# Performance work log

Hardware: AMD Instinct MI355X
Metric: run time of the kernel (lower is better)

The kernel has to match this reference:

```python
import jax, jax.numpy as jnp
import numpy as np

B, H, W, C = 16, 256, 256, 16
HO, WO = 256, 256


def setup_inputs() -> dict:
    key = jax.random.key(0)
    k1, k2 = jax.random.split(key)
    x = jax.random.normal(k1, (B, H, W, C), dtype=jnp.float32)
    # loc network: global avg pool -> dense(C, 6); small weights, identity bias
    W_loc = jax.random.normal(k2, (C, 6), dtype=jnp.float32) * 0.01
    b_loc = jnp.asarray([1.0, 0.0, 0.0, 1.0, 0.0, 0.0], dtype=jnp.float32)
    # coords_grid = np.indices(output_grid_shape): (2, HO, WO), [0]=row idx, [1]=col idx
    coords_grid = jnp.asarray(np.indices((HO, WO), dtype=np.float32))
    return {"x": x, "W_loc": W_loc, "b_loc": b_loc, "coords_grid": coords_grid}


def _forward(x, W_loc, b_loc, coords_grid):
    # loc network: predict 6 affine params per batch element
    pooled = jnp.mean(x, axis=(1, 2))              # [B, C]
    params = pooled @ W_loc + b_loc                # [B, 6]
    A = params[:, :4].reshape(-1, 2, 2)            # [B, 2, 2]
    t = params[:, 4:]                              # [B, 2]
    # grid_transform_fn: affine map of pixel coordinates
    tc = jnp.einsum('bij,jhw->bihw', A, coords_grid) + t[:, :, None, None]  # [B,2,HO,WO]
    yc, xc = tc[:, 0], tc[:, 1]                    # [B, HO, WO] each
    # interpolation_fn: bilinear sampling with clipping (wrap=False)
    y0 = jnp.floor(yc)
    x0 = jnp.floor(xc)
    wy = yc - y0                                   # fractional weights
    wx = xc - x0
    y0i = jnp.clip(y0.astype(jnp.int32), 0, H - 1)
    y1i = jnp.clip(y0.astype(jnp.int32) + 1, 0, H - 1)
    x0i = jnp.clip(x0.astype(jnp.int32), 0, W - 1)
    x1i = jnp.clip(x0.astype(jnp.int32) + 1, 0, W - 1)
    bidx = jnp.arange(x.shape[0])[:, None, None]   # [B,1,1] batch gather index
    Ia = x[bidx, y0i, x0i]                         # [B,HO,WO,C]
    Ib = x[bidx, y0i, x1i]
    Ic = x[bidx, y1i, x0i]
    Id = x[bidx, y1i, x1i]
    wa = ((1.0 - wy) * (1.0 - wx))[..., None]
    wb = ((1.0 - wy) * wx)[..., None]
    wc = (wy * (1.0 - wx))[..., None]
    wd = (wy * wx)[..., None]
    return wa * Ia + wb * Ib + wc * Ic + wd * Id   # [B,HO,WO,C]


def reference(x, W_loc, b_loc, coords_grid):
    return _forward(x, W_loc, b_loc, coords_grid)
```

## Files before the change

kernel.cpp:

```cpp
#include <hip/hip_runtime.h>

#define BB 16
#define HH 256
#define WW 256
#define CC 16
#define NPIX (HH * WW)
#define SLICES 128
#define POOL_BLOCKS (BB * SLICES)
#define SAMPLE_BPB 128
#define SAMPLE_BLOCKS (BB * SAMPLE_BPB)

__global__ __launch_bounds__(256) void pool_partial(const float4* __restrict__ x4,
                                                    float4* __restrict__ part) {
    const int blk = blockIdx.x;
    const int tid = threadIdx.x;
    const float4* p = x4 + (size_t)blk * 2048 + tid;
    float4 acc = {0.f, 0.f, 0.f, 0.f};
#pragma unroll
    for (int k = 0; k < 8; ++k) {
        float4 v = p[k * 256];
        acc.x += v.x; acc.y += v.y; acc.z += v.z; acc.w += v.w;
    }
    for (int off = 4; off < 64; off <<= 1) {
        acc.x += __shfl_down(acc.x, off);
        acc.y += __shfl_down(acc.y, off);
        acc.z += __shfl_down(acc.z, off);
        acc.w += __shfl_down(acc.w, off);
    }
    __shared__ float4 wsum[4][4];
    const int wave = tid >> 6, lane = tid & 63;
    if (lane < 4) wsum[wave][lane] = acc;
    __syncthreads();
    if (tid < 4) {
        float4 t0 = wsum[0][tid], t1 = wsum[1][tid];
        float4 t2 = wsum[2][tid], t3 = wsum[3][tid];
        float4 t;
        t.x = t0.x + t1.x + t2.x + t3.x;
        t.y = t0.y + t1.y + t2.y + t3.y;
        t.z = t0.z + t1.z + t2.z + t3.z;
        t.w = t0.w + t1.w + t2.w + t3.w;
        part[blk * 4 + tid] = t;
    }
}

__global__ __launch_bounds__(256) void sample_fused(
    const float4* __restrict__ x4,
    const float* __restrict__ W_loc,
    const float* __restrict__ b_loc,
    const float4* __restrict__ part,
    float4* __restrict__ out)
{
    const int tid  = threadIdx.x;
    const int blk  = blockIdx.x;
    const int b    = blk >> 7;
    const int wave = tid >> 6, lane = tid & 63;

    __shared__ float4 wsum[4][4];
    __shared__ float  pooled[CC];
    __shared__ float  pr[6];

    {
        const float4* q = part + (size_t)b * 512;
        float4 a0 = q[tid], a1 = q[tid + 256];
        float4 acc;
        acc.x = a0.x + a1.x; acc.y = a0.y + a1.y;
        acc.z = a0.z + a1.z; acc.w = a0.w + a1.w;
        for (int off = 4; off < 64; off <<= 1) {
            acc.x += __shfl_down(acc.x, off);
            acc.y += __shfl_down(acc.y, off);
            acc.z += __shfl_down(acc.z, off);
            acc.w += __shfl_down(acc.w, off);
        }
        if (lane < 4) wsum[wave][lane] = acc;
        __syncthreads();
        if (tid < 4) {
            float4 t0 = wsum[0][tid], t1 = wsum[1][tid];
            float4 t2 = wsum[2][tid], t3 = wsum[3][tid];
            pooled[tid * 4 + 0] = (t0.x + t1.x + t2.x + t3.x) * (1.0f / 65536.0f);
            pooled[tid * 4 + 1] = (t0.y + t1.y + t2.y + t3.y) * (1.0f / 65536.0f);
            pooled[tid * 4 + 2] = (t0.z + t1.z + t2.z + t3.z) * (1.0f / 65536.0f);
            pooled[tid * 4 + 3] = (t0.w + t1.w + t2.w + t3.w) * (1.0f / 65536.0f);
        }
        __syncthreads();
        if (tid < 6) {
            float a = b_loc[tid];
#pragma unroll
            for (int c = 0; c < CC; ++c)
                a += pooled[c] * W_loc[c * 6 + tid];
            pr[tid] = a;
        }
        __syncthreads();
    }

    const float p0 = pr[0], p1 = pr[1], p2 = pr[2];
    const float p3 = pr[3], p4 = pr[4], p5 = pr[5];
    const size_t base    = (size_t)b * NPIX;
    const int    pixBase = (blk & 127) * 512 + (tid >> 2);
    const int    cq      = tid & 3;

#pragma unroll 4
    for (int k = 0; k < 8; ++k) {
        const int pix = pixBase + k * 64;
        const int h = pix >> 8;
        const int w = pix & 255;

        const float fh = (float)h, fw = (float)w;
        const float yc = p0 * fh + p1 * fw + p4;
        const float xc = p2 * fh + p3 * fw + p5;

        const float y0f = floorf(yc), x0f = floorf(xc);
        const float wy = yc - y0f, wx = xc - x0f;
        const int y0 = (int)y0f, x0 = (int)x0f;
        const int y0i = min(max(y0, 0), HH - 1);
        const int y1i = min(max(y0 + 1, 0), HH - 1);
        const int x0i = min(max(x0, 0), WW - 1);
        const int x1i = min(max(x0 + 1, 0), WW - 1);

        const float4* r0 = x4 + (base + (size_t)y0i * WW) * 4 + cq;
        const float4* r1 = x4 + (base + (size_t)y1i * WW) * 4 + cq;
        const float4 Ia = r0[(size_t)x0i * 4];
        const float4 Ib = r0[(size_t)x1i * 4];
        const float4 Ic = r1[(size_t)x0i * 4];
        const float4 Id = r1[(size_t)x1i * 4];

        const float wa = (1.f - wy) * (1.f - wx);
        const float wb = (1.f - wy) * wx;
        const float wc = wy * (1.f - wx);
        const float wd = wy * wx;

        float4 o;
        o.x = wa * Ia.x + wb * Ib.x + wc * Ic.x + wd * Id.x;
        o.y = wa * Ia.y + wb * Ib.y + wc * Ic.y + wd * Id.y;
        o.z = wa * Ia.z + wb * Ib.z + wc * Ic.z + wd * Id.z;
        o.w = wa * Ia.w + wb * Ib.w + wc * Ic.w + wd * Id.w;

        out[(base + pix) * 4 + cq] = o;
    }
}

extern "C" void kernel_launch(void* const* d_in, const int* in_sizes, int n_in,
                              void* d_out, int out_size, void* d_ws, size_t ws_size,
                              hipStream_t stream) {
    const float* x     = (const float*)d_in[0];
    const float* W_loc = (const float*)d_in[1];
    const float* b_loc = (const float*)d_in[2];

    float4* part = (float4*)d_ws;

    pool_partial<<<POOL_BLOCKS, 256, 0, stream>>>((const float4*)x, part);
    sample_fused<<<SAMPLE_BLOCKS, 256, 0, stream>>>((const float4*)x, W_loc, b_loc,
                                                    part, (float4*)d_out);
}
```

Baseline: 129.9 us.

## Stage source rows in LDS for bilinear sampling when row span is small

Each sampling block covers two output rows. It now computes the range of input rows those rows map to, and when the range is at most four rows it copies them into 64KB of dynamic LDS with coalesced loads, then gathers the four taps from LDS instead of global memory. Blocks with a wider range keep the old global-gather path. This adds an extra sync and a large LDS allocation that limits occupancy, and the launch bounds now ask for two blocks per CU. With near-identity transforms the staged rows closely match rows the gathers would hit anyway, so the saving over L2-cached gathers may be small.

```diff
diff --git a/kernel.cpp b/kernel.cpp
--- a/kernel.cpp
+++ b/kernel.cpp
@@ -9,6 +9,7 @@
 #define POOL_BLOCKS (BB * SLICES)
 #define SAMPLE_BPB 128
 #define SAMPLE_BLOCKS (BB * SAMPLE_BPB)
+#define MAXR 4
 
 __global__ __launch_bounds__(256) void pool_partial(const float4* __restrict__ x4,
                                                     float4* __restrict__ part) {
@@ -43,21 +44,23 @@
     }
 }
 
-__global__ __launch_bounds__(256) void sample_fused(
+__global__ __launch_bounds__(256, 2) void sample_fused(
     const float4* __restrict__ x4,
     const float* __restrict__ W_loc,
     const float* __restrict__ b_loc,
     const float4* __restrict__ part,
     float4* __restrict__ out)
 {
+    extern __shared__ float lds_f[];
+    float4* ldsRows = (float4*)lds_f;
+    float4* wsum    = (float4*)lds_f;
+    float*  pooled  = lds_f + 64;
+    float*  prs     = lds_f + 80;
+
     const int tid  = threadIdx.x;
     const int blk  = blockIdx.x;
     const int b    = blk >> 7;
     const int wave = tid >> 6, lane = tid & 63;
-
-    __shared__ float4 wsum[4][4];
-    __shared__ float  pooled[CC];
-    __shared__ float  pr[6];
 
     {
         const float4* q = part + (size_t)b * 512;
@@ -71,11 +74,11 @@
             acc.z += __shfl_down(acc.z, off);
             acc.w += __shfl_down(acc.w, off);
         }
-        if (lane < 4) wsum[wave][lane] = acc;
+        if (lane < 4) wsum[wave * 4 + lane] = acc;
         __syncthreads();
         if (tid < 4) {
-            float4 t0 = wsum[0][tid], t1 = wsum[1][tid];
-            float4 t2 = wsum[2][tid], t3 = wsum[3][tid];
+            float4 t0 = wsum[0 * 4 + tid], t1 = wsum[1 * 4 + tid];
+            float4 t2 = wsum[2 * 4 + tid], t3 = wsum[3 * 4 + tid];
             pooled[tid * 4 + 0] = (t0.x + t1.x + t2.x + t3.x) * (1.0f / 65536.0f);
             pooled[tid * 4 + 1] = (t0.y + t1.y + t2.y + t3.y) * (1.0f / 65536.0f);
             pooled[tid * 4 + 2] = (t0.z + t1.z + t2.z + t3.z) * (1.0f / 65536.0f);
@@ -87,54 +90,113 @@
 #pragma unroll
             for (int c = 0; c < CC; ++c)
                 a += pooled[c] * W_loc[c * 6 + tid];
-            pr[tid] = a;
-        }
-        __syncthreads();
-    }
-
-    const float p0 = pr[0], p1 = pr[1], p2 = pr[2];
-    const float p3 = pr[3], p4 = pr[4], p5 = pr[5];
+            prs[tid] = a;
+        }
+        __syncthreads();
+    }
+
+    const float p0 = prs[0], p1 = prs[1], p2 = prs[2];
+    const float p3 = prs[3], p4 = prs[4], p5 = prs[5];
+    __syncthreads();
+
     const size_t base    = (size_t)b * NPIX;
-    const int    pixBase = (blk & 127) * 512 + (tid >> 2);
+    const int    local   = blk & 127;
+    const int    h0      = local * 2;
+    const int    pixBase = local * 512 + (tid >> 2);
     const int    cq      = tid & 3;
 
+    const float yc00 = p0 * (float)h0       + p4;
+    const float yc01 = p0 * (float)h0       + p1 * 255.f + p4;
+    const float yc10 = p0 * (float)(h0 + 1) + p4;
+    const float yc11 = p0 * (float)(h0 + 1) + p1 * 255.f + p4;
+    const float ymn = fminf(fminf(yc00, yc01), fminf(yc10, yc11));
+    const float ymx = fmaxf(fmaxf(yc00, yc01), fmaxf(yc10, yc11));
+    const int y_lo = min(max((int)floorf(ymn), 0), HH - 1);
+    const int y_hi = min(max((int)floorf(ymx) + 1, 0), HH - 1);
+    const int NR   = y_hi - y_lo + 1;
+
+    if (NR <= MAXR) {
+        const float4* src = x4 + (base + (size_t)y_lo * WW) * 4;
+        const int nf4 = NR * 1024;
+        for (int i = tid; i < nf4; i += 256)
+            ldsRows[i] = src[i];
+        __syncthreads();
+
 #pragma unroll 4
-    for (int k = 0; k < 8; ++k) {
-        const int pix = pixBase + k * 64;
-        const int h = pix >> 8;
-        const int w = pix & 255;
-
-        const float fh = (float)h, fw = (float)w;
-        const float yc = p0 * fh + p1 * fw + p4;
-        const float xc = p2 * fh + p3 * fw + p5;
-
-        const float y0f = floorf(yc), x0f = floorf(xc);
-        const float wy = yc - y0f, wx = xc - x0f;
-        const int y0 = (int)y0f, x0 = (int)x0f;
-        const int y0i = min(max(y0, 0), HH - 1);
-        const int y1i = min(max(y0 + 1, 0), HH - 1);
-        const int x0i = min(max(x0, 0), WW - 1);
-        const int x1i = min(max(x0 + 1, 0), WW - 1);
-
-        const float4* r0 = x4 + (base + (size_t)y0i * WW) * 4 + cq;
-        const float4* r1 = x4 + (base + (size_t)y1i * WW) * 4 + cq;
-        const float4 Ia = r0[(size_t)x0i * 4];
-        const float4 Ib = r0[(size_t)x1i * 4];
-        const float4 Ic = r1[(size_t)x0i * 4];
-        const float4 Id = r1[(size_t)x1i * 4];
-
-        const float wa = (1.f - wy) * (1.f - wx);
-        const float wb = (1.f - wy) * wx;
-        const float wc = wy * (1.f - wx);
-        const float wd = wy * wx;
-
-        float4 o;
-        o.x = wa * Ia.x + wb * Ib.x + wc * Ic.x + wd * Id.x;
-        o.y = wa * Ia.y + wb * Ib.y + wc * Ic.y + wd * Id.y;
-        o.z = wa * Ia.z + wb * Ib.z + wc * Ic.z + wd * Id.z;
-        o.w = wa * Ia.w + wb * Ib.w + wc * Ic.w + wd * Id.w;
-
-        out[(base + pix) * 4 + cq] = o;
+        for (int k = 0; k < 8; ++k) {
+            const int pix = pixBase + k * 64;
+            const int h = pix >> 8;
+            const int w = pix & 255;
+
+            const float fh = (float)h, fw = (float)w;
+            const float yc = p0 * fh + p1 * fw + p4;
+            const float xc = p2 * fh + p3 * fw + p5;
+
+            const float y0f = floorf(yc), x0f = floorf(xc);
+            const float wy = yc - y0f, wx = xc - x0f;
+            const int y0 = (int)y0f, x0 = (int)x0f;
+            const int s0  = min(max(y0, 0), HH - 1) - y_lo;
+            const int s1  = min(max(y0 + 1, 0), HH - 1) - y_lo;
+            const int x0i = min(max(x0, 0), WW - 1);
+            const int x1i = min(max(x0 + 1, 0), WW - 1);
+
+            const float4 Ia = ldsRows[s0 * 1024 + x0i * 4 + cq];
+            const float4 Ib = ldsRows[s0 * 1024 + x1i * 4 + cq];
+            const float4 Ic = ldsRows[s1 * 1024 + x0i * 4 + cq];
+            const float4 Id = ldsRows[s1 * 1024 + x1i * 4 + cq];
+
+            const float wa = (1.f - wy) * (1.f - wx);
+            const float wb = (1.f - wy) * wx;
+            const float wc = wy * (1.f - wx);
+            const float wd = wy * wx;
+
+            float4 o;
+            o.x = wa * Ia.x + wb * Ib.x + wc * Ic.x + wd * Id.x;
+            o.y = wa * Ia.y + wb * Ib.y + wc * Ic.y + wd * Id.y;
+            o.z = wa * Ia.z + wb * Ib.z + wc * Ic.z + wd * Id.z;
+            o.w = wa * Ia.w + wb * Ib.w + wc * Ic.w + wd * Id.w;
+
+            out[(base + pix) * 4 + cq] = o;
+        }
+    } else {
+#pragma unroll 4
+        for (int k = 0; k < 8; ++k) {
+            const int pix = pixBase + k * 64;
+            const int h = pix >> 8;
+            const int w = pix & 255;
+
+            const float fh = (float)h, fw = (float)w;
+            const float yc = p0 * fh + p1 * fw + p4;
+            const float xc = p2 * fh + p3 * fw + p5;
+
+            const float y0f = floorf(yc), x0f = floorf(xc);
+            const float wy = yc - y0f, wx = xc - x0f;
+            const int y0 = (int)y0f, x0 = (int)x0f;
+            const int y0i = min(max(y0, 0), HH - 1);
+            const int y1i = min(max(y0 + 1, 0), HH - 1);
+            const int x0i = min(max(x0, 0), WW - 1);
+            const int x1i = min(max(x0 + 1, 0), WW - 1);
+
+            const float4* r0 = x4 + (base + (size_t)y0i * WW) * 4 + cq;
+            const float4* r1 = x4 + (base + (size_t)y1i * WW) * 4 + cq;
+            const float4 Ia = r0[(size_t)x0i * 4];
+            const float4 Ib = r0[(size_t)x1i * 4];
+            const float4 Ic = r1[(size_t)x0i * 4];
+            const float4 Id = r1[(size_t)x1i * 4];
+
+            const float wa = (1.f - wy) * (1.f - wx);
+            const float wb = (1.f - wy) * wx;
+            const float wc = wy * (1.f - wx);
+            const float wd = wy * wx;
+
+            float4 o;
+            o.x = wa * Ia.x + wb * Ib.x + wc * Ic.x + wd * Id.x;
+            o.y = wa * Ia.y + wb * Ib.y + wc * Ic.y + wd * Id.y;
+            o.z = wa * Ia.z + wb * Ib.z + wc * Ic.z + wd * Id.z;
+            o.w = wa * Ia.w + wb * Ib.w + wc * Ic.w + wd * Id.w;
+
+            out[(base + pix) * 4 + cq] = o;
+        }
     }
 }
 
@@ -148,6 +210,6 @@
     float4* part = (float4*)d_ws;
 
     pool_partial<<<POOL_BLOCKS, 256, 0, stream>>>((const float4*)x, part);
-    sample_fused<<<SAMPLE_BLOCKS, 256, 0, stream>>>((const float4*)x, W_loc, b_loc,
-                                                    part, (float4*)d_out);
+    sample_fused<<<SAMPLE_BLOCKS, 256, MAXR * 16384, stream>>>(
+        (const float4*)x, W_loc, b_loc, part, (float4*)d_out);
 }
```

Result: slower. 140.2 us (+7.9%).
